# Kernel optimization log

Measured on AMD Instinct MI355X. Metric: run time of the kernel, lower is better.

Reference implementation:

```python
import jax, jax.numpy as jnp
import numpy as np

EMBED = 1024
HEADS = 16
B, T = 4, 2048


def setup_inputs() -> dict:
    key = jax.random.key(0)
    k1, k2, k3, k4, k5 = jax.random.split(key, 5)
    s_in = 1.0 / np.sqrt(EMBED)
    return {
        "x": jax.random.normal(k1, (B, T, EMBED), dtype=jnp.float32),
        "w_qkv": jax.random.uniform(k2, (3 * EMBED, EMBED), jnp.float32, -s_in, s_in),
        "b_qkv": jax.random.uniform(k3, (3 * EMBED,), jnp.float32, -s_in, s_in),
        "w_proj": jax.random.uniform(k4, (EMBED, EMBED), jnp.float32, -s_in, s_in),
        "b_proj": jax.random.uniform(k5, (EMBED,), jnp.float32, -s_in, s_in),
    }


def reference(x, w_qkv, b_qkv, w_proj, b_proj):
    Bz, Tz, C = x.shape
    nh = HEADS
    hs = C // nh
    qkv = jnp.einsum('btc,oc->bto', x, w_qkv) + b_qkv  # [B,T,3C]
    q, k, v = jnp.split(qkv, 3, axis=-1)
    # [B, nh, T, hs]
    q = q.reshape(Bz, Tz, nh, hs).transpose(0, 2, 1, 3)
    k = k.reshape(Bz, Tz, nh, hs).transpose(0, 2, 1, 3)
    v = v.reshape(Bz, Tz, nh, hs).transpose(0, 2, 1, 3)
    scale = 1.0 / np.sqrt(hs).astype(np.float32)
    att = jnp.einsum('bhqd,bhkd->bhqk', q, k) * scale
    causal_mask = jnp.tril(jnp.ones((Tz, Tz), dtype=bool))
    att = jnp.where(causal_mask[None, None], att, jnp.finfo(att.dtype).min)
    att = jax.nn.softmax(att, axis=-1)
    y = jnp.einsum('bhqk,bhkd->bhqd', att, v)
    y = y.transpose(0, 2, 1, 3).reshape(Bz, Tz, C)
    return jnp.einsum('btc,oc->bto', y, w_proj) + b_proj
```

## Files before the change

kernel.cpp:

```cpp
#include <hip/hip_runtime.h>

typedef __bf16 bf16x8 __attribute__((ext_vector_type(8)));
typedef float f32x4 __attribute__((ext_vector_type(4)));

#define DI __device__ __forceinline__

#define WAIT_VMCNT(N)                                        \
  do {                                                       \
    __builtin_amdgcn_sched_barrier(0);                       \
    asm volatile("s_waitcnt vmcnt(" #N ")" ::: "memory");    \
    __builtin_amdgcn_sched_barrier(0);                       \
  } while (0)

DI unsigned short f2bf(float f) {
  unsigned int u = __float_as_uint(f);
  u += 0x7FFFu + ((u >> 16) & 1u);
  return (unsigned short)(u >> 16);
}

DI unsigned cvt_pk_bf16(float a, float b) {
  unsigned r;
  asm("v_cvt_pk_bf16_f32 %0, %1, %2" : "=v"(r) : "v"(a), "v"(b));
  return r;
}

DI float exp2_fast(float x) {
  float r;
  asm("v_exp_f32 %0, %1" : "=v"(r) : "v"(x));
  return r;
}

DI void fence() { asm volatile("" ::: "memory"); }
DI void bar() { fence(); __builtin_amdgcn_s_barrier(); fence(); }

DI bf16x8 ld16(const void* p) {
  union { uint4 u; bf16x8 b; } c;
  c.u = *reinterpret_cast<const uint4*>(p);
  return c.b;
}

DI f32x4 mfma16(bf16x8 a, bf16x8 b, f32x4 c) {
  return __builtin_amdgcn_mfma_f32_16x16x32_bf16(a, b, c, 0, 0, 0);
}

DI void gload_lds16(const void* g, void* l) {
  __builtin_amdgcn_global_load_lds(
      (const __attribute__((address_space(1))) unsigned int*)g,
      (__attribute__((address_space(3))) unsigned int*)l, 16, 0, 0);
}

__global__ void cvt_all(const float* __restrict__ x, const float* __restrict__ wq,
                        const float* __restrict__ wp,
                        unsigned short* __restrict__ xb, unsigned short* __restrict__ wqb,
                        unsigned short* __restrict__ wpb) {
  int i = blockIdx.x * blockDim.x + threadIdx.x;
  const float* s;
  unsigned short* d;
  int off;
  if (i < 2097152) { s = x; d = xb; off = i; }
  else if (i < 2097152 + 786432) { s = wq; d = wqb; off = i - 2097152; }
  else { s = wp; d = wpb; off = i - (2097152 + 786432); }
  float4 v = reinterpret_cast<const float4*>(s)[off];
  uint2 o;
  o.x = cvt_pk_bf16(v.x, v.y);
  o.y = cvt_pk_bf16(v.z, v.w);
  reinterpret_cast<uint2*>(d)[off] = o;
}

template <int N, int MODE>
__global__ __launch_bounds__(256)
void gemm_bt(const unsigned short* __restrict__ A,
             const unsigned short* __restrict__ W,
             const float* __restrict__ bias,
             float* __restrict__ out,
             unsigned short* __restrict__ qo,
             unsigned short* __restrict__ ko,
             unsigned short* __restrict__ vo) {
  constexpr int K = 1024;
  __shared__ __align__(16) char smem[32768];
  char* Asm = smem;
  char* Bsm = smem + 16384;
  const int tid = threadIdx.x;
  const int ln = tid & 63;
  const int w  = tid >> 6;
  const int wm = w >> 1, wn = w & 1;
  const int g = ln >> 4, q = ln & 15;
  const int m0 = blockIdx.x * 128;
  const int n0 = blockIdx.y * 128;

  f32x4 acc[4][4] = {};

  for (int kt = 0; kt < K / 64; ++kt) {
    if (kt) bar();
#pragma unroll
    for (int i = 0; i < 4; ++i) {
      const int chunk = i * 4 + w;
      const int o = chunk * 1024 + ln * 16;
      const int row = o >> 7;
      const int colb = (o & 127) ^ ((row & 7) << 4);
      gload_lds16((const char*)A + ((size_t)(m0 + row) * K + kt * 64) * 2 + colb,
                  Asm + chunk * 1024);
      gload_lds16((const char*)W + ((size_t)(n0 + row) * K + kt * 64) * 2 + colb,
                  Bsm + chunk * 1024);
    }
    WAIT_VMCNT(0);
    bar();
#pragma unroll
    for (int ks = 0; ks < 2; ++ks) {
      bf16x8 av[4], bv[4];
#pragma unroll
      for (int mf = 0; mf < 4; ++mf) {
        const int row = wm * 64 + mf * 16 + q;
        av[mf] = ld16(Asm + ((row * 128 + ks * 64 + g * 16) ^ ((row & 7) << 4)));
      }
#pragma unroll
      for (int nf = 0; nf < 4; ++nf) {
        const int row = wn * 64 + nf * 16 + q;
        bv[nf] = ld16(Bsm + ((row * 128 + ks * 64 + g * 16) ^ ((row & 7) << 4)));
      }
#pragma unroll
      for (int mf = 0; mf < 4; ++mf)
#pragma unroll
        for (int nf = 0; nf < 4; ++nf)
          acc[mf][nf] = mfma16(av[mf], bv[nf], acc[mf][nf]);
    }
  }

#pragma unroll
  for (int nf = 0; nf < 4; ++nf) {
    const int col = n0 + wn * 64 + nf * 16 + q;
    const float bv = bias[col];
#pragma unroll
    for (int mf = 0; mf < 4; ++mf) {
      const int rbase = m0 + wm * 64 + mf * 16 + g * 4;
      if constexpr (MODE == 0) {
#pragma unroll
        for (int r = 0; r < 4; ++r)
          out[(size_t)(rbase + r) * N + col] = acc[mf][nf][r] + bv;
      } else {
        const int b = rbase >> 11, t0 = rbase & 2047;
        if (col < 1024) {
          const int h = col >> 6, d = col & 63;
          unsigned short* qp = qo + ((((size_t)b * 16 + h) << 11) + t0) * 64 + d;
#pragma unroll
          for (int r = 0; r < 4; ++r)
            qp[r * 64] = f2bf((acc[mf][nf][r] + bv) * 0.18033688011112042f);
        } else if (col < 2048) {
          const int c = col - 1024;
          const int h = c >> 6, d = c & 63;
          unsigned short* kp = ko + ((((size_t)b * 16 + h) << 11) + t0) * 64 + d;
#pragma unroll
          for (int r = 0; r < 4; ++r)
            kp[r * 64] = f2bf(acc[mf][nf][r] + bv);
        } else {
          const int c = col - 2048;
          const int h = c >> 6, d = c & 63;
          uint2 pk;
          pk.x = cvt_pk_bf16(acc[mf][nf][0] + bv, acc[mf][nf][1] + bv);
          pk.y = cvt_pk_bf16(acc[mf][nf][2] + bv, acc[mf][nf][3] + bv);
          *(uint2*)(vo + ((((size_t)b * 16 + h) << 6) + d) * 2048 + t0) = pk;
        }
      }
    }
  }
}

DI int asb(int row) { return ((row & 3) | (((row >> 3) & 1) << 2)) << 4; }

__global__ __launch_bounds__(256, 4)
void attn_fwd(const unsigned short* __restrict__ Qb,
              const unsigned short* __restrict__ Kb,
              const unsigned short* __restrict__ Vtb,
              unsigned short* __restrict__ Yb) {
  __shared__ __align__(16) char smem[32768];
  const int tid = threadIdx.x;
  const int ln = tid & 63;
  const int w = tid >> 6;
  const int g = ln >> 4, q = ln & 15;
  const int bh = blockIdx.x;
  const int pair = blockIdx.y;
  const size_t base = (size_t)bh * 2048 * 64;
  const int b = bh >> 4, h = bh & 15;
  const int qrow = (q & 3) + 8 * (q >> 2);

  auto stage = [&](int j, int buf) {
    char* Kd = smem + buf * 16384;
    char* Vd = Kd + 8192;
    const int kv0 = j << 6;
    const char* Kg = (const char*)(Kb + base + (size_t)kv0 * 64);
    const char* Vg = (const char*)(Vtb + base) + kv0 * 2;
#pragma unroll
    for (int i = 0; i < 2; ++i) {
      const int chunk = i * 4 + w;
      const int o = chunk * 1024 + ln * 16;
      const int row = o >> 7;
      const int colb = (o & 127) ^ asb(row);
      gload_lds16(Kg + row * 128 + colb, Kd + chunk * 1024);
      gload_lds16(Vg + (size_t)row * 4096 + colb, Vd + chunk * 1024);
    }
  };

  auto run_qtile = [&](int qt) {
    const int q0 = qt * 64;
    const int qw = q0 + w * 16;

    bf16x8 qf[2];
#pragma unroll
    for (int kf = 0; kf < 2; ++kf)
      qf[kf] = ld16(Qb + base + (size_t)(qw + q) * 64 + kf * 32 + g * 8);
    WAIT_VMCNT(0);

    float m_run = -INFINITY;
    float l_run = 0.f;
    f32x4 yt[4] = {};

    const int nkv = qt + 1;
    stage(0, 0);
    for (int j = 0; j < nkv; ++j) {
      if (j + 1 < nkv) {
        stage(j + 1, (j + 1) & 1);
        WAIT_VMCNT(4);
      } else {
        WAIT_VMCNT(0);
      }
      bar();

      const int kv0 = j << 6;
      const char* Ksm = smem + (j & 1) * 16384;
      const char* Vsm = Ksm + 8192;
      f32x4 st[4] = {};
      __builtin_amdgcn_s_setprio(1);
#pragma unroll
      for (int f = 0; f < 4; ++f) {
        const int row = qrow + 4 * (f & 1) + 32 * (f >> 1);
        const int swz = asb(row);
        const bf16x8 a0 = ld16(Ksm + ((row * 128 + g * 16) ^ swz));
        const bf16x8 a1 = ld16(Ksm + ((row * 128 + 64 + g * 16) ^ swz));
        st[f] = mfma16(a0, qf[0], st[f]);
        st[f] = mfma16(a1, qf[1], st[f]);
      }
      __builtin_amdgcn_s_setprio(0);
      if (kv0 + 63 > qw) {
#pragma unroll
        for (int f = 0; f < 4; ++f) {
          const int kvb = kv0 + 8 * g + 4 * (f & 1) + 32 * (f >> 1);
#pragma unroll
          for (int r = 0; r < 4; ++r)
            if (kvb + r > qw + q) st[f][r] = -INFINITY;
        }
      }
      {
        float vmax = -INFINITY;
#pragma unroll
        for (int f = 0; f < 4; ++f) {
          const f32x4 v = st[f];
          vmax = fmaxf(fmaxf(vmax, fmaxf(v[0], v[1])), fmaxf(v[2], v[3]));
        }
        vmax = fmaxf(vmax, __shfl_xor(vmax, 16));
        vmax = fmaxf(vmax, __shfl_xor(vmax, 32));
        const float mo = m_run;
        if (__any(vmax > mo)) {
          const float mn = fmaxf(mo, vmax);
          const float corr = exp2_fast(mo - mn);
          m_run = mn;
          l_run *= corr;
#pragma unroll
          for (int mfd = 0; mfd < 4; ++mfd) yt[mfd] *= corr;
        }
        const float mcur = m_run;
        float ls = 0.f;
#pragma unroll
        for (int f = 0; f < 4; ++f) {
#pragma unroll
          for (int r = 0; r < 4; ++r) {
            st[f][r] = exp2_fast(st[f][r] - mcur);
            ls += st[f][r];
          }
        }
        ls += __shfl_xor(ls, 16);
        ls += __shfl_xor(ls, 32);
        l_run += ls;
      }
      union { uint4 u; bf16x8 b; } pb0, pb1;
      pb0.u.x = cvt_pk_bf16(st[0][0], st[0][1]);
      pb0.u.y = cvt_pk_bf16(st[0][2], st[0][3]);
      pb0.u.z = cvt_pk_bf16(st[1][0], st[1][1]);
      pb0.u.w = cvt_pk_bf16(st[1][2], st[1][3]);
      pb1.u.x = cvt_pk_bf16(st[2][0], st[2][1]);
      pb1.u.y = cvt_pk_bf16(st[2][2], st[2][3]);
      pb1.u.z = cvt_pk_bf16(st[3][0], st[3][1]);
      pb1.u.w = cvt_pk_bf16(st[3][2], st[3][3]);
      __builtin_amdgcn_s_setprio(1);
#pragma unroll
      for (int mfd = 0; mfd < 4; ++mfd) {
        const int vrow = mfd * 16 + q;
        const int swz = asb(vrow);
        const bf16x8 v0 = ld16(Vsm + ((vrow * 128 + g * 16) ^ swz));
        const bf16x8 v1 = ld16(Vsm + ((vrow * 128 + 64 + g * 16) ^ swz));
        yt[mfd] = mfma16(v0, pb0.b, yt[mfd]);
        yt[mfd] = mfma16(v1, pb1.b, yt[mfd]);
      }
      __builtin_amdgcn_s_setprio(0);
      bar();
    }

    const float inv = 1.f / l_run;
    const int qr = qw + q;
    unsigned short* yp = Yb + (size_t)(b * 2048 + qr) * 1024 + h * 64;
#pragma unroll
    for (int mfd = 0; mfd < 4; ++mfd) {
      uint2 o2;
      o2.x = cvt_pk_bf16(yt[mfd][0] * inv, yt[mfd][1] * inv);
      o2.y = cvt_pk_bf16(yt[mfd][2] * inv, yt[mfd][3] * inv);
      *(uint2*)(yp + mfd * 16 + g * 4) = o2;
    }
  };

  run_qtile(31 - pair);
  run_qtile(pair);
}

extern "C" void kernel_launch(void* const* d_in, const int* in_sizes, int n_in,
                              void* d_out, int out_size, void* d_ws, size_t ws_size,
                              hipStream_t stream) {
  const float* x      = (const float*)d_in[0];
  const float* w_qkv  = (const float*)d_in[1];
  const float* b_qkv  = (const float*)d_in[2];
  const float* w_proj = (const float*)d_in[3];
  const float* b_proj = (const float*)d_in[4];
  float* out = (float*)d_out;
  char* ws = (char*)d_ws;

  unsigned short* xb  = (unsigned short*)(ws);
  unsigned short* wqb = (unsigned short*)(ws + (size_t)(16 << 20));
  unsigned short* wpb = (unsigned short*)(ws + (size_t)(22 << 20));
  unsigned short* Qb  = (unsigned short*)(ws + (size_t)(24 << 20));
  unsigned short* Kb  = (unsigned short*)(ws + (size_t)(40 << 20));
  unsigned short* Vtb = (unsigned short*)(ws + (size_t)(56 << 20));
  unsigned short* Yb  = (unsigned short*)(ws + (size_t)(72 << 20));

  cvt_all<<<12288, 256, 0, stream>>>(x, w_qkv, w_proj, xb, wqb, wpb);
  gemm_bt<3072, 1><<<dim3(64, 24), 256, 0, stream>>>(xb, wqb, b_qkv, nullptr, Qb, Kb, Vtb);
  attn_fwd<<<dim3(64, 16), 256, 0, stream>>>(Qb, Kb, Vtb, Yb);
  gemm_bt<1024, 0><<<dim3(64, 8), 256, 0, stream>>>(Yb, wpb, b_proj, out, nullptr, nullptr, nullptr);
}
```

Measured before the change: 164.0 us.

## Share K/V tile loads between paired high and low query tiles

The block previously processed its two query tiles (31-pair and pair) one after another, reloading K/V tiles from global memory for each. Now both tiles run in one KV loop: each staged K/V tile is consumed by the high tile and also by the low tile while j <= lo. This cuts global K/V traffic and barrier rounds for the shared prefix. In exchange, register pressure rises from holding two sets of accumulators and softmax state, which may lower occupancy.

```diff
diff --git a/kernel.cpp b/kernel.cpp
--- a/kernel.cpp
+++ b/kernel.cpp
@@ -200,110 +200,84 @@
     }
   };
 
-  auto run_qtile = [&](int qt) {
-    const int q0 = qt * 64;
-    const int qw = q0 + w * 16;
-
-    bf16x8 qf[2];
-#pragma unroll
-    for (int kf = 0; kf < 2; ++kf)
-      qf[kf] = ld16(Qb + base + (size_t)(qw + q) * 64 + kf * 32 + g * 8);
-    WAIT_VMCNT(0);
-
-    float m_run = -INFINITY;
-    float l_run = 0.f;
-    f32x4 yt[4] = {};
-
-    const int nkv = qt + 1;
-    stage(0, 0);
-    for (int j = 0; j < nkv; ++j) {
-      if (j + 1 < nkv) {
-        stage(j + 1, (j + 1) & 1);
-        WAIT_VMCNT(4);
-      } else {
-        WAIT_VMCNT(0);
-      }
-      bar();
-
-      const int kv0 = j << 6;
-      const char* Ksm = smem + (j & 1) * 16384;
-      const char* Vsm = Ksm + 8192;
-      f32x4 st[4] = {};
-      __builtin_amdgcn_s_setprio(1);
+  auto tile_step = [&](const bf16x8* qf, float& m_run, float& l_run, f32x4* yt,
+                       int qw, int kv0, const char* Ksm, const char* Vsm) {
+    f32x4 st[4] = {};
+    __builtin_amdgcn_s_setprio(1);
+#pragma unroll
+    for (int f = 0; f < 4; ++f) {
+      const int row = qrow + 4 * (f & 1) + 32 * (f >> 1);
+      const int swz = asb(row);
+      const bf16x8 a0 = ld16(Ksm + ((row * 128 + g * 16) ^ swz));
+      const bf16x8 a1 = ld16(Ksm + ((row * 128 + 64 + g * 16) ^ swz));
+      st[f] = mfma16(a0, qf[0], st[f]);
+      st[f] = mfma16(a1, qf[1], st[f]);
+    }
+    __builtin_amdgcn_s_setprio(0);
+    if (kv0 + 63 > qw) {
 #pragma unroll
       for (int f = 0; f < 4; ++f) {
-        const int row = qrow + 4 * (f & 1) + 32 * (f >> 1);
-        const int swz = asb(row);
-        const bf16x8 a0 = ld16(Ksm + ((row * 128 + g * 16) ^ swz));
-        const bf16x8 a1 = ld16(Ksm + ((row * 128 + 64 + g * 16) ^ swz));
-        st[f] = mfma16(a0, qf[0], st[f]);
-        st[f] = mfma16(a1, qf[1], st[f]);
-      }
-      __builtin_amdgcn_s_setprio(0);
-      if (kv0 + 63 > qw) {
-#pragma unroll
-        for (int f = 0; f < 4; ++f) {
-          const int kvb = kv0 + 8 * g + 4 * (f & 1) + 32 * (f >> 1);
-#pragma unroll
-          for (int r = 0; r < 4; ++r)
-            if (kvb + r > qw + q) st[f][r] = -INFINITY;
+        const int kvb = kv0 + 8 * g + 4 * (f & 1) + 32 * (f >> 1);
+#pragma unroll
+        for (int r = 0; r < 4; ++r)
+          if (kvb + r > qw + q) st[f][r] = -INFINITY;
+      }
+    }
+    {
+      float vmax = -INFINITY;
+#pragma unroll
+      for (int f = 0; f < 4; ++f) {
+        const f32x4 v = st[f];
+        vmax = fmaxf(fmaxf(vmax, fmaxf(v[0], v[1])), fmaxf(v[2], v[3]));
+      }
+      vmax = fmaxf(vmax, __shfl_xor(vmax, 16));
+      vmax = fmaxf(vmax, __shfl_xor(vmax, 32));
+      const float mo = m_run;
+      if (__any(vmax > mo)) {
+        const float mn = fmaxf(mo, vmax);
+        const float corr = exp2_fast(mo - mn);
+        m_run = mn;
+        l_run *= corr;
+#pragma unroll
+        for (int mfd = 0; mfd < 4; ++mfd) yt[mfd] *= corr;
+      }
+      const float mcur = m_run;
+      float ls = 0.f;
+#pragma unroll
+      for (int f = 0; f < 4; ++f) {
+#pragma unroll
+        for (int r = 0; r < 4; ++r) {
+          st[f][r] = exp2_fast(st[f][r] - mcur);
+          ls += st[f][r];
         }
       }
-      {
-        float vmax = -INFINITY;
-#pragma unroll
-        for (int f = 0; f < 4; ++f) {
-          const f32x4 v = st[f];
-          vmax = fmaxf(fmaxf(vmax, fmaxf(v[0], v[1])), fmaxf(v[2], v[3]));
-        }
-        vmax = fmaxf(vmax, __shfl_xor(vmax, 16));
-        vmax = fmaxf(vmax, __shfl_xor(vmax, 32));
-        const float mo = m_run;
-        if (__any(vmax > mo)) {
-          const float mn = fmaxf(mo, vmax);
-          const float corr = exp2_fast(mo - mn);
-          m_run = mn;
-          l_run *= corr;
-#pragma unroll
-          for (int mfd = 0; mfd < 4; ++mfd) yt[mfd] *= corr;
-        }
-        const float mcur = m_run;
-        float ls = 0.f;
-#pragma unroll
-        for (int f = 0; f < 4; ++f) {
-#pragma unroll
-          for (int r = 0; r < 4; ++r) {
-            st[f][r] = exp2_fast(st[f][r] - mcur);
-            ls += st[f][r];
-          }
-        }
-        ls += __shfl_xor(ls, 16);
-        ls += __shfl_xor(ls, 32);
-        l_run += ls;
-      }
-      union { uint4 u; bf16x8 b; } pb0, pb1;
-      pb0.u.x = cvt_pk_bf16(st[0][0], st[0][1]);
-      pb0.u.y = cvt_pk_bf16(st[0][2], st[0][3]);
-      pb0.u.z = cvt_pk_bf16(st[1][0], st[1][1]);
-      pb0.u.w = cvt_pk_bf16(st[1][2], st[1][3]);
-      pb1.u.x = cvt_pk_bf16(st[2][0], st[2][1]);
-      pb1.u.y = cvt_pk_bf16(st[2][2], st[2][3]);
-      pb1.u.z = cvt_pk_bf16(st[3][0], st[3][1]);
-      pb1.u.w = cvt_pk_bf16(st[3][2], st[3][3]);
-      __builtin_amdgcn_s_setprio(1);
-#pragma unroll
-      for (int mfd = 0; mfd < 4; ++mfd) {
-        const int vrow = mfd * 16 + q;
-        const int swz = asb(vrow);
-        const bf16x8 v0 = ld16(Vsm + ((vrow * 128 + g * 16) ^ swz));
-        const bf16x8 v1 = ld16(Vsm + ((vrow * 128 + 64 + g * 16) ^ swz));
-        yt[mfd] = mfma16(v0, pb0.b, yt[mfd]);
-        yt[mfd] = mfma16(v1, pb1.b, yt[mfd]);
-      }
-      __builtin_amdgcn_s_setprio(0);
-      bar();
-    }
-
+      ls += __shfl_xor(ls, 16);
+      ls += __shfl_xor(ls, 32);
+      l_run += ls;
+    }
+    union { uint4 u; bf16x8 bb; } pb0, pb1;
+    pb0.u.x = cvt_pk_bf16(st[0][0], st[0][1]);
+    pb0.u.y = cvt_pk_bf16(st[0][2], st[0][3]);
+    pb0.u.z = cvt_pk_bf16(st[1][0], st[1][1]);
+    pb0.u.w = cvt_pk_bf16(st[1][2], st[1][3]);
+    pb1.u.x = cvt_pk_bf16(st[2][0], st[2][1]);
+    pb1.u.y = cvt_pk_bf16(st[2][2], st[2][3]);
+    pb1.u.z = cvt_pk_bf16(st[3][0], st[3][1]);
+    pb1.u.w = cvt_pk_bf16(st[3][2], st[3][3]);
+    __builtin_amdgcn_s_setprio(1);
+#pragma unroll
+    for (int mfd = 0; mfd < 4; ++mfd) {
+      const int vrow = mfd * 16 + q;
+      const int swz = asb(vrow);
+      const bf16x8 v0 = ld16(Vsm + ((vrow * 128 + g * 16) ^ swz));
+      const bf16x8 v1 = ld16(Vsm + ((vrow * 128 + 64 + g * 16) ^ swz));
+      yt[mfd] = mfma16(v0, pb0.bb, yt[mfd]);
+      yt[mfd] = mfma16(v1, pb1.bb, yt[mfd]);
+    }
+    __builtin_amdgcn_s_setprio(0);
+  };
+
+  auto epilogue = [&](float l_run, const f32x4* yt, int qw) {
     const float inv = 1.f / l_run;
     const int qr = qw + q;
     unsigned short* yp = Yb + (size_t)(b * 2048 + qr) * 1024 + h * 64;
@@ -316,8 +290,43 @@
     }
   };
 
-  run_qtile(31 - pair);
-  run_qtile(pair);
+  const int hi = 31 - pair, lo = pair;
+  const int qw_hi = hi * 64 + w * 16;
+  const int qw_lo = lo * 64 + w * 16;
+
+  bf16x8 qh[2], ql[2];
+#pragma unroll
+  for (int kf = 0; kf < 2; ++kf) {
+    qh[kf] = ld16(Qb + base + (size_t)(qw_hi + q) * 64 + kf * 32 + g * 8);
+    ql[kf] = ld16(Qb + base + (size_t)(qw_lo + q) * 64 + kf * 32 + g * 8);
+  }
+  WAIT_VMCNT(0);
+
+  float m_hi = -INFINITY, l_hi = 0.f, m_lo = -INFINITY, l_lo = 0.f;
+  f32x4 yh[4] = {}, yl[4] = {};
+
+  const int njv = hi + 1;
+  stage(0, 0);
+  for (int j = 0; j < njv; ++j) {
+    if (j + 1 < njv) {
+      stage(j + 1, (j + 1) & 1);
+      WAIT_VMCNT(4);
+    } else {
+      WAIT_VMCNT(0);
+    }
+    bar();
+
+    const int kv0 = j << 6;
+    const char* Ksm = smem + (j & 1) * 16384;
+    const char* Vsm = Ksm + 8192;
+    tile_step(qh, m_hi, l_hi, yh, qw_hi, kv0, Ksm, Vsm);
+    if (j <= lo)
+      tile_step(ql, m_lo, l_lo, yl, qw_lo, kv0, Ksm, Vsm);
+    bar();
+  }
+
+  epilogue(l_hi, yh, qw_hi);
+  epilogue(l_lo, yl, qw_lo);
 }
 
 extern "C" void kernel_launch(void* const* d_in, const int* in_sizes, int n_in,
```

Result: no change. 160.8 us, median of 4 (-1.9%).
